# Kernel tuning notes

Hardware: AMD Instinct MI355X
Metric: run time of the kernel (lower is better)

Reference implementation:

```python
import jax, jax.numpy as jnp
import numpy as np

D_MODEL = 1024
NUM_HEADS = 16
HEAD_DIM = D_MODEL // NUM_HEADS


def setup_inputs() -> dict:
    key = jax.random.key(0)
    ks = jax.random.split(key, 5)
    scale = 1.0 / np.sqrt(D_MODEL)
    x = jax.random.normal(ks[0], (2, 2048, D_MODEL), dtype=jnp.float32)
    Wqkv = jax.random.normal(ks[1], (D_MODEL, 3 * D_MODEL), dtype=jnp.float32) * scale
    bqkv = jax.random.normal(ks[2], (3 * D_MODEL,), dtype=jnp.float32) * 0.02
    Wout = jax.random.normal(ks[3], (D_MODEL, D_MODEL), dtype=jnp.float32) * scale
    bout = jax.random.normal(ks[4], (D_MODEL,), dtype=jnp.float32) * 0.02
    return {"x": x, "Wqkv": Wqkv, "bqkv": bqkv, "Wout": Wout, "bout": bout}


def reference(x, Wqkv, bqkv, Wout, bout):
    B, T, D = x.shape
    H, Hd = NUM_HEADS, HEAD_DIM
    # fused QKV projection: [B,T,3D] -> [3,B,H,T,Hd]
    qkv = (x @ Wqkv + bqkv).reshape(B, T, 3, H, Hd).transpose(2, 0, 3, 1, 4)
    q, k, v = qkv[0], qkv[1], qkv[2]
    # scaled dot-product attention with full TxT scores (faithful to source)
    scores = jnp.einsum("bhqd,bhkd->bhqk", q, k) / np.sqrt(Hd).astype(np.float32)
    weights = jax.nn.softmax(scores, axis=-1)
    context = jnp.einsum("bhqk,bhkd->bhqd", weights, v)
    context = context.transpose(0, 2, 1, 3).reshape(B, T, D)
    return context @ Wout + bout
```

## Files before the change

kernel.cpp:

```cpp
#include <hip/hip_runtime.h>
#include <hip/hip_bf16.h>

#define D_MODEL 1024
#define T_SEQ   2048
#define BATCH   2
#define NHEADS  16
#define HDIM    64
#define QKVSZ   (BATCH * NHEADS * T_SEQ * HDIM)

#define SCALE_Q 0.18033688011112042f

typedef __bf16 bf16_t;
typedef bf16_t bf16x8  __attribute__((ext_vector_type(8)));
typedef float  f32x4   __attribute__((ext_vector_type(4)));
typedef float  f32x16  __attribute__((ext_vector_type(16)));
typedef unsigned uint32x4 __attribute__((ext_vector_type(4)));

#if __has_builtin(__builtin_amdgcn_exp2f)
#define EXP2F(x) __builtin_amdgcn_exp2f(x)
#else
#define EXP2F(x) exp2f(x)
#endif

__device__ __forceinline__ unsigned short f2bf(float f) {
    union { float f; unsigned u; } v; v.f = f;
    unsigned u = v.u;
    u += 0x7FFFu + ((u >> 16) & 1u);
    return (unsigned short)(u >> 16);
}

__device__ __forceinline__ unsigned pkbf(float a, float b) {
    unsigned r;
    asm("v_cvt_pk_bf16_f32 %0, %1, %2" : "=v"(r) : "v"(a), "v"(b));
    return r;
}

__device__ __forceinline__ void gload16(const unsigned short* g, unsigned short* l) {
    __builtin_amdgcn_global_load_lds(
        (const __attribute__((address_space(1))) void*)g,
        (__attribute__((address_space(3))) void*)l,
        16, 0, 0);
}

__global__ void cvt_f32_bf16(const float* __restrict__ src,
                             unsigned short* __restrict__ dst, int n4) {
    int i = blockIdx.x * blockDim.x + threadIdx.x;
    if (i < n4) {
        float4 v = reinterpret_cast<const float4*>(src)[i];
        ushort4 o;
        o.x = f2bf(v.x); o.y = f2bf(v.y); o.z = f2bf(v.z); o.w = f2bf(v.w);
        reinterpret_cast<ushort4*>(dst)[i] = o;
    }
}

__global__ __launch_bounds__(256) void cvt_transpose(
    const float* __restrict__ src, unsigned short* __restrict__ dst, int K, int N)
{
    __shared__ unsigned short Ls[64][72];
    const int n0 = blockIdx.x * 64, k0 = blockIdx.y * 64;
    const int tid = threadIdx.x;
    #pragma unroll
    for (int it = 0; it < 4; ++it) {
        const int r = it * 16 + (tid >> 4);
        const int c = (tid & 15) * 4;
        float4 v = *reinterpret_cast<const float4*>(src + (size_t)(k0 + r) * N + n0 + c);
        Ls[c + 0][r] = f2bf(v.x); Ls[c + 1][r] = f2bf(v.y);
        Ls[c + 2][r] = f2bf(v.z); Ls[c + 3][r] = f2bf(v.w);
    }
    __syncthreads();
    #pragma unroll
    for (int it = 0; it < 2; ++it) {
        const int rn = it * 32 + (tid >> 3);
        const int ck = (tid & 7) * 8;
        *reinterpret_cast<uint4*>(dst + (size_t)(n0 + rn) * K + k0 + ck) =
            *reinterpret_cast<const uint4*>(&Ls[rn][ck]);
    }
}

__global__ __launch_bounds__(256) void transpose_v(
    const unsigned short* __restrict__ v, unsigned short* __restrict__ vt)
{
    __shared__ unsigned short Ls[64][72];
    const int t0 = blockIdx.x * 64;
    const size_t base = ((size_t)(blockIdx.z * NHEADS + blockIdx.y)) * T_SEQ * HDIM;
    const int tid = threadIdx.x;
    const int r  = tid >> 2;
    const int c0 = (tid & 3) * 16;
    unsigned short tmp[16];
    *reinterpret_cast<uint4*>(&tmp[0]) =
        *reinterpret_cast<const uint4*>(v + base + (size_t)(t0 + r) * HDIM + c0);
    *reinterpret_cast<uint4*>(&tmp[8]) =
        *reinterpret_cast<const uint4*>(v + base + (size_t)(t0 + r) * HDIM + c0 + 8);
    #pragma unroll
    for (int i = 0; i < 16; ++i) Ls[c0 + i][r] = tmp[i];
    __syncthreads();
    const int rn = tid >> 2;
    const int ck = (tid & 3) * 16;
    const int a  = ck >> 4;
    const int kb = 32 * (a >> 1) + 16 * (a & 1);
    unsigned short buf[16];
    #pragma unroll
    for (int i = 0; i < 16; ++i) {
        const int key = kb + 4 * (i >> 3) + 8 * ((i & 7) >> 2) + (i & 3);
        buf[i] = Ls[rn][key];
    }
    *reinterpret_cast<uint4*>(vt + base + (size_t)rn * T_SEQ + t0 + ck) =
        *reinterpret_cast<const uint4*>(&buf[0]);
    *reinterpret_cast<uint4*>(vt + base + (size_t)rn * T_SEQ + t0 + ck + 8) =
        *reinterpret_cast<const uint4*>(&buf[8]);
}

template<int MODE>
__global__ __launch_bounds__(256) void gemm128(
    const unsigned short* __restrict__ A,
    const unsigned short* __restrict__ BT,
    const float* __restrict__ bias,
    unsigned short* __restrict__ qkv,
    float* __restrict__ outf,
    int M, int N, int K)
{
    __shared__ unsigned short As[2][128 * 32];
    __shared__ unsigned short Bs[2][128 * 32];
    const int tid = threadIdx.x, wv = tid >> 6, lane = tid & 63;
    const int wr = wv >> 1, wc = wv & 1;
    const int m0 = blockIdx.y * 128, n0 = blockIdx.x * 128;

    const int srow0 = 32 * wv + (lane >> 2);
    const int skc0  = (lane & 3) ^ ((srow0 >> 1) & 3);
    const int srow1 = srow0 + 16;
    const int skc1  = (lane & 3) ^ ((srow1 >> 1) & 3);

    #define GSTAGE(k0v, bf)                                                     \
        {                                                                       \
            gload16(A  + (size_t)(m0 + srow0) * K + (k0v) + skc0 * 8,           \
                    &As[bf][(32 * wv) * 32]);                                   \
            gload16(BT + (size_t)(n0 + srow0) * K + (k0v) + skc0 * 8,           \
                    &Bs[bf][(32 * wv) * 32]);                                   \
            gload16(A  + (size_t)(m0 + srow1) * K + (k0v) + skc1 * 8,           \
                    &As[bf][(32 * wv + 16) * 32]);                              \
            gload16(BT + (size_t)(n0 + srow1) * K + (k0v) + skc1 * 8,           \
                    &Bs[bf][(32 * wv + 16) * 32]);                              \
        }

    f32x4 acc[4][4] = {};

    GSTAGE(0, 0);
    __syncthreads();

    const int nk = K >> 5;
    for (int k = 0; k < nk; ++k) {
        const int cur = k & 1;
        if (k + 1 < nk) GSTAGE((k + 1) << 5, cur ^ 1);

        bf16x8 af[4], bfr[4];
        #pragma unroll
        for (int m = 0; m < 4; ++m) {
            const int row = 64 * wr + 16 * m + (lane & 15);
            const int s   = (lane >> 4) ^ ((row >> 1) & 3);
            af[m] = *reinterpret_cast<const bf16x8*>(&As[cur][row * 32 + s * 8]);
        }
        #pragma unroll
        for (int n = 0; n < 4; ++n) {
            const int row = 64 * wc + 16 * n + (lane & 15);
            const int s   = (lane >> 4) ^ ((row >> 1) & 3);
            bfr[n] = *reinterpret_cast<const bf16x8*>(&Bs[cur][row * 32 + s * 8]);
        }
        #pragma unroll
        for (int m = 0; m < 4; ++m)
            #pragma unroll
            for (int n = 0; n < 4; ++n)
                acc[m][n] = __builtin_amdgcn_mfma_f32_16x16x32_bf16(af[m], bfr[n], acc[m][n], 0, 0, 0);
        __syncthreads();
    }
    #undef GSTAGE

    const int rb = m0 + 64 * wr + ((lane >> 4) << 2);
    const int cb = n0 + 64 * wc + (lane & 15);
    #pragma unroll
    for (int n = 0; n < 4; ++n) {
        const int c = cb + 16 * n;
        const float bc = bias[c];
        #pragma unroll
        for (int m = 0; m < 4; ++m) {
            #pragma unroll
            for (int jr = 0; jr < 4; ++jr) {
                const int r = rb + 16 * m + jr;
                float val = acc[m][n][jr] + bc;
                if (MODE == 0) {
                    const int which = c >> 10;
                    const int rem = c & 1023;
                    const int h = rem >> 6, hd = rem & 63;
                    const int b = r >> 11, t = r & 2047;
                    if (which == 0) val *= SCALE_Q;
                    qkv[(size_t)which * QKVSZ + ((((size_t)b * NHEADS + h) * T_SEQ + t) << 6) + hd] = f2bf(val);
                } else {
                    outf[(size_t)r * N + c] = val;
                }
            }
        }
    }
}

__global__ __launch_bounds__(512) void attn32(
    const unsigned short* __restrict__ qb,
    const unsigned short* __restrict__ kb,
    const unsigned short* __restrict__ vtb,
    unsigned short* __restrict__ ctx)
{
    __shared__ unsigned short Ks[2][2][64 * 64];
    __shared__ unsigned short Vt[2][2][64 * 64];

    const int tid = threadIdx.x;
    const int wv = tid >> 6, lane = tid & 63;
    const int wg = wv >> 2, wl = wv & 3;
    const int ql = lane & 31;
    const int hi = lane >> 5;

    const int P    = blockIdx.x + 16 * blockIdx.y + 256 * blockIdx.z;
    const int xcd  = P & 7, slot = P >> 3;
    const int qt   = slot & 15;
    const int hidx = xcd * 4 + (slot >> 4);
    const int h    = hidx & 15, b = hidx >> 4;

    const size_t base = ((size_t)(b * NHEADS + h)) * T_SEQ * HDIM;
    const unsigned short* Kp  = kb  + base;
    const unsigned short* Vtp = vtb + base;
    const unsigned short* Qp  = qb  + base + ((size_t)qt * 128 + wl * 32 + ql) * HDIM;

    const bf16x8 qf0 = *reinterpret_cast<const bf16x8*>(Qp + 0  + hi * 8);
    const bf16x8 qf1 = *reinterpret_cast<const bf16x8*>(Qp + 16 + hi * 8);
    const bf16x8 qf2 = *reinterpret_cast<const bf16x8*>(Qp + 32 + hi * 8);
    const bf16x8 qf3 = *reinterpret_cast<const bf16x8*>(Qp + 48 + hi * 8);

    const int srow = lane >> 3;
    const int ssl  = lane & 7;
    #define STAGE(i, bf)                                                          \
        {                                                                         \
            _Pragma("unroll")                                                     \
            for (int ihalf = 0; ihalf < 2; ++ihalf) {                             \
                const int g2  = wl * 2 + ihalf;                                   \
                const int row = 8 * g2 + srow;                                    \
                const int sl  = ssl ^ (row & 7) ^ ((row >> 3) & 3);               \
                gload16(Kp  + (size_t)((wg * 16 + (i)) * 64 + row) * HDIM + sl * 8, \
                        &Ks[wg][bf][g2 * 512]);                                   \
                gload16(Vtp + (size_t)row * T_SEQ + (wg * 16 + (i)) * 64 + sl * 8, \
                        &Vt[wg][bf][g2 * 512]);                                   \
            }                                                                     \
        }

    STAGE(0, 0);
    __syncthreads();

    const int kx = (ql & 7) ^ ((ql >> 3) & 3);

    float m = -1e30f, l = 0.f;
    f32x16 o0 = {}, o1 = {};

    for (int i = 0; i < 16; ++i) {
        const int cur = i & 1;
        if (i + 1 < 16) STAGE(i + 1, cur ^ 1);

        f32x16 s0 = {}, s1 = {};
        __builtin_amdgcn_s_setprio(1);
        #pragma unroll
        for (int c = 0; c < 4; ++c) {
            const int sw = (2 * c + hi) ^ kx;
            const bf16x8 k0 = *reinterpret_cast<const bf16x8*>(&Ks[wg][cur][(ql)      * 64 + sw * 8]);
            const bf16x8 k1 = *reinterpret_cast<const bf16x8*>(&Ks[wg][cur][(32 + ql) * 64 + sw * 8]);
            const bf16x8 qc = (c == 0) ? qf0 : (c == 1) ? qf1 : (c == 2) ? qf2 : qf3;
            s0 = __builtin_amdgcn_mfma_f32_32x32x16_bf16(k0, qc, s0, 0, 0, 0);
            s1 = __builtin_amdgcn_mfma_f32_32x32x16_bf16(k1, qc, s1, 0, 0, 0);
        }
        __builtin_amdgcn_s_setprio(0);

        float a0 = fmaxf(s0[0], s0[4]), a1 = fmaxf(s0[1], s0[5]);
        float a2 = fmaxf(s0[2], s0[6]), a3 = fmaxf(s0[3], s0[7]);
        a0 = fmaxf(a0, fmaxf(s0[8],  s0[12]));  a1 = fmaxf(a1, fmaxf(s0[9],  s0[13]));
        a2 = fmaxf(a2, fmaxf(s0[10], s0[14])); a3 = fmaxf(a3, fmaxf(s0[11], s0[15]));
        a0 = fmaxf(a0, fmaxf(s1[0], s1[4]));   a1 = fmaxf(a1, fmaxf(s1[1], s1[5]));
        a2 = fmaxf(a2, fmaxf(s1[2], s1[6]));   a3 = fmaxf(a3, fmaxf(s1[3], s1[7]));
        a0 = fmaxf(a0, fmaxf(s1[8],  s1[12])); a1 = fmaxf(a1, fmaxf(s1[9],  s1[13]));
        a2 = fmaxf(a2, fmaxf(s1[10], s1[14])); a3 = fmaxf(a3, fmaxf(s1[11], s1[15]));
        float mx = fmaxf(fmaxf(a0, a1), fmaxf(a2, a3));
        mx = fmaxf(mx, __shfl_xor(mx, 32));

        if (__any(mx > m + 8.0f)) {
            const float mn = fmaxf(m, mx);
            const float sc = EXP2F(m - mn);
            l *= sc; m = mn;
            #pragma unroll
            for (int r = 0; r < 16; ++r) { o0[r] *= sc; o1[r] *= sc; }
        }

        #pragma unroll
        for (int r = 0; r < 16; ++r) s0[r] = EXP2F(s0[r] - m);
        #pragma unroll
        for (int r = 0; r < 16; ++r) s1[r] = EXP2F(s1[r] - m);
        float b0 = 0.f, b1 = 0.f, b2 = 0.f, b3 = 0.f;
        #pragma unroll
        for (int r = 0; r < 16; r += 4) {
            b0 += s0[r]; b1 += s0[r + 1]; b2 += s0[r + 2]; b3 += s0[r + 3];
            b0 += s1[r]; b1 += s1[r + 1]; b2 += s1[r + 2]; b3 += s1[r + 3];
        }
        float rs = (b0 + b1) + (b2 + b3);
        l += rs + __shfl_xor(rs, 32);

        __builtin_amdgcn_s_setprio(1);
        #pragma unroll
        for (int kc = 0; kc < 4; ++kc) {
            uint32x4 fw;
            if (kc == 0) {
                fw.x = pkbf(s0[0], s0[1]);   fw.y = pkbf(s0[2], s0[3]);
                fw.z = pkbf(s0[4], s0[5]);   fw.w = pkbf(s0[6], s0[7]);
            } else if (kc == 1) {
                fw.x = pkbf(s0[8], s0[9]);   fw.y = pkbf(s0[10], s0[11]);
                fw.z = pkbf(s0[12], s0[13]); fw.w = pkbf(s0[14], s0[15]);
            } else if (kc == 2) {
                fw.x = pkbf(s1[0], s1[1]);   fw.y = pkbf(s1[2], s1[3]);
                fw.z = pkbf(s1[4], s1[5]);   fw.w = pkbf(s1[6], s1[7]);
            } else {
                fw.x = pkbf(s1[8], s1[9]);   fw.y = pkbf(s1[10], s1[11]);
                fw.z = pkbf(s1[12], s1[13]); fw.w = pkbf(s1[14], s1[15]);
            }
            const bf16x8 pa = __builtin_bit_cast(bf16x8, fw);
            const int sw = (2 * kc + hi) ^ kx;
            const bf16x8 vva = *reinterpret_cast<const bf16x8*>(&Vt[wg][cur][(ql)      * 64 + sw * 8]);
            const bf16x8 vvb = *reinterpret_cast<const bf16x8*>(&Vt[wg][cur][(32 + ql) * 64 + sw * 8]);
            o0 = __builtin_amdgcn_mfma_f32_32x32x16_bf16(vva, pa, o0, 0, 0, 0);
            o1 = __builtin_amdgcn_mfma_f32_32x32x16_bf16(vvb, pa, o1, 0, 0, 0);
        }
        __builtin_amdgcn_s_setprio(0);

        __syncthreads();
    }
    #undef STAGE

    float* xo0  = (float*)&Ks[0][0][0];
    float* xo1m = (float*)&Vt[0][0][0];
    const int idx = wl * 64 + lane;
    if (wg == 1) {
        float* pa0 = xo0 + idx * 17;
        float* pb0 = xo1m + idx * 19;
        #pragma unroll
        for (int r = 0; r < 16; ++r) pa0[r] = o0[r];
        #pragma unroll
        for (int r = 0; r < 16; ++r) pb0[r] = o1[r];
        pb0[16] = m; pb0[17] = l;
    }
    __syncthreads();
    if (wg == 0) {
        const float* pa0 = xo0 + idx * 17;
        const float* pb0 = xo1m + idx * 19;
        const float m2 = pb0[16], l2 = pb0[17];
        const float mn = fmaxf(m, m2);
        const float ca = EXP2F(m - mn), cb = EXP2F(m2 - mn);
        const float invl = 1.0f / (l * ca + l2 * cb);
        const float fa = ca * invl, fb = cb * invl;

        const int t = qt * 128 + wl * 32 + ql;
        unsigned short* crow = ctx + ((size_t)b * T_SEQ + t) * D_MODEL + h * HDIM;
        #pragma unroll
        for (int r4 = 0; r4 < 4; ++r4) {
            const int d0 = 8 * r4 + 4 * hi;
            ushort4 w;
            w.x = f2bf(o0[4 * r4 + 0] * fa + pa0[4 * r4 + 0] * fb);
            w.y = f2bf(o0[4 * r4 + 1] * fa + pa0[4 * r4 + 1] * fb);
            w.z = f2bf(o0[4 * r4 + 2] * fa + pa0[4 * r4 + 2] * fb);
            w.w = f2bf(o0[4 * r4 + 3] * fa + pa0[4 * r4 + 3] * fb);
            *reinterpret_cast<ushort4*>(crow + d0) = w;
            w.x = f2bf(o1[4 * r4 + 0] * fa + pb0[4 * r4 + 0] * fb);
            w.y = f2bf(o1[4 * r4 + 1] * fa + pb0[4 * r4 + 1] * fb);
            w.z = f2bf(o1[4 * r4 + 2] * fa + pb0[4 * r4 + 2] * fb);
            w.w = f2bf(o1[4 * r4 + 3] * fa + pb0[4 * r4 + 3] * fb);
            *reinterpret_cast<ushort4*>(crow + 32 + d0) = w;
        }
    }
}

extern "C" void kernel_launch(void* const* d_in, const int* in_sizes, int n_in,
                              void* d_out, int out_size, void* d_ws, size_t ws_size,
                              hipStream_t stream) {
    const float* x    = (const float*)d_in[0];
    const float* Wqkv = (const float*)d_in[1];
    const float* bqkv = (const float*)d_in[2];
    const float* Wout = (const float*)d_in[3];
    const float* bout = (const float*)d_in[4];
    float* out = (float*)d_out;

    char* ws = (char*)d_ws;
    unsigned short* xb    = (unsigned short*)(ws);
    unsigned short* wqkvT = (unsigned short*)(ws + 8388608);
    unsigned short* woutT = (unsigned short*)(ws + 14680064);
    unsigned short* qkv   = (unsigned short*)(ws + 16777216);
    unsigned short* ctx   = (unsigned short*)(ws + 41943040);

    int n4 = (BATCH * T_SEQ * D_MODEL) / 4;
    cvt_f32_bf16<<<(n4 + 255) / 256, 256, 0, stream>>>(x, xb, n4);

    dim3 gt1(3 * D_MODEL / 64, D_MODEL / 64);
    cvt_transpose<<<gt1, 256, 0, stream>>>(Wqkv, wqkvT, D_MODEL, 3 * D_MODEL);
    dim3 gt2(D_MODEL / 64, D_MODEL / 64);
    cvt_transpose<<<gt2, 256, 0, stream>>>(Wout, woutT, D_MODEL, D_MODEL);

    dim3 g1(3 * D_MODEL / 128, (BATCH * T_SEQ) / 128);
    gemm128<0><<<g1, 256, 0, stream>>>(xb, wqkvT, bqkv, qkv, nullptr,
                                       BATCH * T_SEQ, 3 * D_MODEL, D_MODEL);

    dim3 gtv(T_SEQ / 64, NHEADS, BATCH);
    transpose_v<<<gtv, 256, 0, stream>>>(qkv + (size_t)2 * QKVSZ, xb);

    dim3 g2(T_SEQ / 128, NHEADS, BATCH);
    attn32<<<g2, 512, 0, stream>>>(qkv,
                                   qkv + (size_t)QKVSZ,
                                   xb,
                                   ctx);

    dim3 g3(D_MODEL / 128, (BATCH * T_SEQ) / 128);
    gemm128<1><<<g3, 256, 0, stream>>>(ctx, woutT, bout, nullptr, out,
                                       BATCH * T_SEQ, D_MODEL, D_MODEL);
}
```

Measured before the change: 130.9 us.

## Software-pipeline QK and softmax across iterations with staggered wave groups

The attention loop is restructured so the QK^T MFMA for the next key tile overlaps the softmax and PV of the current tile. K is prefetched two tiles ahead and V one tile ahead, and the two wave groups run softmax and QK in opposite orders so MFMA and VALU work interleave. Q is now staged in shared memory instead of held in registers, and the launch bound asks for 4 blocks per CU. This aims to hide softmax latency behind matrix work, at the cost of extra LDS traffic for Q and more register pressure from the double score buffers.

```diff
diff --git a/kernel.cpp b/kernel.cpp
--- a/kernel.cpp
+++ b/kernel.cpp
@@ -201,7 +201,7 @@
     }
 }
 
-__global__ __launch_bounds__(512) void attn32(
+__global__ __launch_bounds__(512, 4) void attn32(
     const unsigned short* __restrict__ qb,
     const unsigned short* __restrict__ kb,
     const unsigned short* __restrict__ vtb,
@@ -209,6 +209,7 @@
 {
     __shared__ unsigned short Ks[2][2][64 * 64];
     __shared__ unsigned short Vt[2][2][64 * 64];
+    __shared__ unsigned short Qs[128 * 64];
 
     const int tid = threadIdx.x;
     const int wv = tid >> 6, lane = tid & 63;
@@ -225,115 +226,154 @@
     const size_t base = ((size_t)(b * NHEADS + h)) * T_SEQ * HDIM;
     const unsigned short* Kp  = kb  + base;
     const unsigned short* Vtp = vtb + base;
-    const unsigned short* Qp  = qb  + base + ((size_t)qt * 128 + wl * 32 + ql) * HDIM;
-
-    const bf16x8 qf0 = *reinterpret_cast<const bf16x8*>(Qp + 0  + hi * 8);
-    const bf16x8 qf1 = *reinterpret_cast<const bf16x8*>(Qp + 16 + hi * 8);
-    const bf16x8 qf2 = *reinterpret_cast<const bf16x8*>(Qp + 32 + hi * 8);
-    const bf16x8 qf3 = *reinterpret_cast<const bf16x8*>(Qp + 48 + hi * 8);
+    const unsigned short* Qt  = qb  + base + (size_t)qt * 128 * HDIM;
 
     const int srow = lane >> 3;
     const int ssl  = lane & 7;
-    #define STAGE(i, bf)                                                          \
+
+    #define STAGE_K(i, bf)                                                        \
         {                                                                         \
             _Pragma("unroll")                                                     \
             for (int ihalf = 0; ihalf < 2; ++ihalf) {                             \
                 const int g2  = wl * 2 + ihalf;                                   \
                 const int row = 8 * g2 + srow;                                    \
                 const int sl  = ssl ^ (row & 7) ^ ((row >> 3) & 3);               \
-                gload16(Kp  + (size_t)((wg * 16 + (i)) * 64 + row) * HDIM + sl * 8, \
+                gload16(Kp + (size_t)((wg * 16 + (i)) * 64 + row) * HDIM + sl * 8,\
                         &Ks[wg][bf][g2 * 512]);                                   \
-                gload16(Vtp + (size_t)row * T_SEQ + (wg * 16 + (i)) * 64 + sl * 8, \
+            }                                                                     \
+        }
+    #define STAGE_V(i, bf)                                                        \
+        {                                                                         \
+            _Pragma("unroll")                                                     \
+            for (int ihalf = 0; ihalf < 2; ++ihalf) {                             \
+                const int g2  = wl * 2 + ihalf;                                   \
+                const int row = 8 * g2 + srow;                                    \
+                const int sl  = ssl ^ (row & 7) ^ ((row >> 3) & 3);               \
+                gload16(Vtp + (size_t)row * T_SEQ + (wg * 16 + (i)) * 64 + sl * 8,\
                         &Vt[wg][bf][g2 * 512]);                                   \
             }                                                                     \
         }
 
-    STAGE(0, 0);
+    {
+        #pragma unroll
+        for (int ihalf = 0; ihalf < 2; ++ihalf) {
+            const int g2  = wv * 2 + ihalf;
+            const int row = 8 * g2 + srow;
+            const int sl  = ssl ^ (row & 7) ^ ((row >> 3) & 3);
+            gload16(Qt + (size_t)row * HDIM + sl * 8, &Qs[g2 * 512]);
+        }
+    }
+    STAGE_K(0, 0); STAGE_V(0, 0); STAGE_K(1, 1);
     __syncthreads();
 
     const int kx = (ql & 7) ^ ((ql >> 3) & 3);
 
+    #define QK_MFMA(SOUT0, SOUT1, NXT)                                            \
+        {                                                                         \
+            __builtin_amdgcn_s_setprio(1);                                        \
+            _Pragma("unroll")                                                     \
+            for (int c = 0; c < 4; ++c) {                                         \
+                const int sw = (2 * c + hi) ^ kx;                                 \
+                const bf16x8 k0 = *reinterpret_cast<const bf16x8*>(&Ks[wg][NXT][(ql)      * 64 + sw * 8]); \
+                const bf16x8 k1 = *reinterpret_cast<const bf16x8*>(&Ks[wg][NXT][(32 + ql) * 64 + sw * 8]); \
+                const bf16x8 qc = *reinterpret_cast<const bf16x8*>(&Qs[(wl * 32 + ql) * 64 + sw * 8]);     \
+                SOUT0 = __builtin_amdgcn_mfma_f32_32x32x16_bf16(k0, qc, SOUT0, 0, 0, 0); \
+                SOUT1 = __builtin_amdgcn_mfma_f32_32x32x16_bf16(k1, qc, SOUT1, 0, 0, 0); \
+            }                                                                     \
+            __builtin_amdgcn_s_setprio(0);                                        \
+        }
+
+    #define SOFTMAX_PACK(SIN0, SIN1)                                             \
+        {                                                                         \
+            float a0 = fmaxf(SIN0[0], SIN0[4]), a1 = fmaxf(SIN0[1], SIN0[5]);     \
+            float a2 = fmaxf(SIN0[2], SIN0[6]), a3 = fmaxf(SIN0[3], SIN0[7]);     \
+            a0 = fmaxf(a0, fmaxf(SIN0[8],  SIN0[12])); a1 = fmaxf(a1, fmaxf(SIN0[9],  SIN0[13])); \
+            a2 = fmaxf(a2, fmaxf(SIN0[10], SIN0[14])); a3 = fmaxf(a3, fmaxf(SIN0[11], SIN0[15])); \
+            a0 = fmaxf(a0, fmaxf(SIN1[0], SIN1[4]));   a1 = fmaxf(a1, fmaxf(SIN1[1], SIN1[5]));   \
+            a2 = fmaxf(a2, fmaxf(SIN1[2], SIN1[6]));   a3 = fmaxf(a3, fmaxf(SIN1[3], SIN1[7]));   \
+            a0 = fmaxf(a0, fmaxf(SIN1[8],  SIN1[12])); a1 = fmaxf(a1, fmaxf(SIN1[9],  SIN1[13])); \
+            a2 = fmaxf(a2, fmaxf(SIN1[10], SIN1[14])); a3 = fmaxf(a3, fmaxf(SIN1[11], SIN1[15])); \
+            float mx = fmaxf(fmaxf(a0, a1), fmaxf(a2, a3));                       \
+            mx = fmaxf(mx, __shfl_xor(mx, 32));                                   \
+            if (__any(mx > m + 8.0f)) {                                           \
+                const float mn = fmaxf(m, mx);                                    \
+                const float sc = EXP2F(m - mn);                                   \
+                l *= sc; m = mn;                                                  \
+                _Pragma("unroll")                                                 \
+                for (int r = 0; r < 16; ++r) { o0[r] *= sc; o1[r] *= sc; }        \
+            }                                                                     \
+            _Pragma("unroll")                                                     \
+            for (int r = 0; r < 16; ++r) SIN0[r] = EXP2F(SIN0[r] - m);            \
+            _Pragma("unroll")                                                     \
+            for (int r = 0; r < 16; ++r) SIN1[r] = EXP2F(SIN1[r] - m);            \
+            float b0 = 0.f, b1 = 0.f, b2 = 0.f, b3 = 0.f;                         \
+            _Pragma("unroll")                                                     \
+            for (int r = 0; r < 16; r += 4) {                                     \
+                b0 += SIN0[r]; b1 += SIN0[r + 1]; b2 += SIN0[r + 2]; b3 += SIN0[r + 3]; \
+                b0 += SIN1[r]; b1 += SIN1[r + 1]; b2 += SIN1[r + 2]; b3 += SIN1[r + 3]; \
+            }                                                                     \
+            float rs = (b0 + b1) + (b2 + b3);                                     \
+            l += rs + __shfl_xor(rs, 32);                                         \
+            pwa.x = pkbf(SIN0[0], SIN0[1]);   pwa.y = pkbf(SIN0[2], SIN0[3]);     \
+            pwa.z = pkbf(SIN0[4], SIN0[5]);   pwa.w = pkbf(SIN0[6], SIN0[7]);     \
+            pwb.x = pkbf(SIN0[8], SIN0[9]);   pwb.y = pkbf(SIN0[10], SIN0[11]);   \
+            pwb.z = pkbf(SIN0[12], SIN0[13]); pwb.w = pkbf(SIN0[14], SIN0[15]);   \
+            pwc.x = pkbf(SIN1[0], SIN1[1]);   pwc.y = pkbf(SIN1[2], SIN1[3]);     \
+            pwc.z = pkbf(SIN1[4], SIN1[5]);   pwc.w = pkbf(SIN1[6], SIN1[7]);     \
+            pwd.x = pkbf(SIN1[8], SIN1[9]);   pwd.y = pkbf(SIN1[10], SIN1[11]);   \
+            pwd.z = pkbf(SIN1[12], SIN1[13]); pwd.w = pkbf(SIN1[14], SIN1[15]);   \
+        }
+
+    #define PV_STEP(PW, KC, CUR)                                                  \
+        {                                                                         \
+            const bf16x8 pa = __builtin_bit_cast(bf16x8, PW);                     \
+            const int sw = (2 * (KC) + hi) ^ kx;                                  \
+            const bf16x8 vva = *reinterpret_cast<const bf16x8*>(&Vt[wg][CUR][(ql)      * 64 + sw * 8]); \
+            const bf16x8 vvb = *reinterpret_cast<const bf16x8*>(&Vt[wg][CUR][(32 + ql) * 64 + sw * 8]); \
+            o0 = __builtin_amdgcn_mfma_f32_32x32x16_bf16(vva, pa, o0, 0, 0, 0);   \
+            o1 = __builtin_amdgcn_mfma_f32_32x32x16_bf16(vvb, pa, o1, 0, 0, 0);   \
+        }
+    #define PV_MFMA(CUR)                                                          \
+        {                                                                         \
+            __builtin_amdgcn_s_setprio(1);                                        \
+            PV_STEP(pwa, 0, CUR); PV_STEP(pwb, 1, CUR);                           \
+            PV_STEP(pwc, 2, CUR); PV_STEP(pwd, 3, CUR);                           \
+            __builtin_amdgcn_s_setprio(0);                                        \
+        }
+
     float m = -1e30f, l = 0.f;
-    f32x16 o0 = {}, o1 = {};
-
-    for (int i = 0; i < 16; ++i) {
-        const int cur = i & 1;
-        if (i + 1 < 16) STAGE(i + 1, cur ^ 1);
-
-        f32x16 s0 = {}, s1 = {};
-        __builtin_amdgcn_s_setprio(1);
-        #pragma unroll
-        for (int c = 0; c < 4; ++c) {
-            const int sw = (2 * c + hi) ^ kx;
-            const bf16x8 k0 = *reinterpret_cast<const bf16x8*>(&Ks[wg][cur][(ql)      * 64 + sw * 8]);
-            const bf16x8 k1 = *reinterpret_cast<const bf16x8*>(&Ks[wg][cur][(32 + ql) * 64 + sw * 8]);
-            const bf16x8 qc = (c == 0) ? qf0 : (c == 1) ? qf1 : (c == 2) ? qf2 : qf3;
-            s0 = __builtin_amdgcn_mfma_f32_32x32x16_bf16(k0, qc, s0, 0, 0, 0);
-            s1 = __builtin_amdgcn_mfma_f32_32x32x16_bf16(k1, qc, s1, 0, 0, 0);
-        }
-        __builtin_amdgcn_s_setprio(0);
-
-        float a0 = fmaxf(s0[0], s0[4]), a1 = fmaxf(s0[1], s0[5]);
-        float a2 = fmaxf(s0[2], s0[6]), a3 = fmaxf(s0[3], s0[7]);
-        a0 = fmaxf(a0, fmaxf(s0[8],  s0[12]));  a1 = fmaxf(a1, fmaxf(s0[9],  s0[13]));
-        a2 = fmaxf(a2, fmaxf(s0[10], s0[14])); a3 = fmaxf(a3, fmaxf(s0[11], s0[15]));
-        a0 = fmaxf(a0, fmaxf(s1[0], s1[4]));   a1 = fmaxf(a1, fmaxf(s1[1], s1[5]));
-        a2 = fmaxf(a2, fmaxf(s1[2], s1[6]));   a3 = fmaxf(a3, fmaxf(s1[3], s1[7]));
-        a0 = fmaxf(a0, fmaxf(s1[8],  s1[12])); a1 = fmaxf(a1, fmaxf(s1[9],  s1[13]));
-        a2 = fmaxf(a2, fmaxf(s1[10], s1[14])); a3 = fmaxf(a3, fmaxf(s1[11], s1[15]));
-        float mx = fmaxf(fmaxf(a0, a1), fmaxf(a2, a3));
-        mx = fmaxf(mx, __shfl_xor(mx, 32));
-
-        if (__any(mx > m + 8.0f)) {
-            const float mn = fmaxf(m, mx);
-            const float sc = EXP2F(m - mn);
-            l *= sc; m = mn;
-            #pragma unroll
-            for (int r = 0; r < 16; ++r) { o0[r] *= sc; o1[r] *= sc; }
-        }
-
-        #pragma unroll
-        for (int r = 0; r < 16; ++r) s0[r] = EXP2F(s0[r] - m);
-        #pragma unroll
-        for (int r = 0; r < 16; ++r) s1[r] = EXP2F(s1[r] - m);
-        float b0 = 0.f, b1 = 0.f, b2 = 0.f, b3 = 0.f;
-        #pragma unroll
-        for (int r = 0; r < 16; r += 4) {
-            b0 += s0[r]; b1 += s0[r + 1]; b2 += s0[r + 2]; b3 += s0[r + 3];
-            b0 += s1[r]; b1 += s1[r + 1]; b2 += s1[r + 2]; b3 += s1[r + 3];
-        }
-        float rs = (b0 + b1) + (b2 + b3);
-        l += rs + __shfl_xor(rs, 32);
-
-        __builtin_amdgcn_s_setprio(1);
-        #pragma unroll
-        for (int kc = 0; kc < 4; ++kc) {
-            uint32x4 fw;
-            if (kc == 0) {
-                fw.x = pkbf(s0[0], s0[1]);   fw.y = pkbf(s0[2], s0[3]);
-                fw.z = pkbf(s0[4], s0[5]);   fw.w = pkbf(s0[6], s0[7]);
-            } else if (kc == 1) {
-                fw.x = pkbf(s0[8], s0[9]);   fw.y = pkbf(s0[10], s0[11]);
-                fw.z = pkbf(s0[12], s0[13]); fw.w = pkbf(s0[14], s0[15]);
-            } else if (kc == 2) {
-                fw.x = pkbf(s1[0], s1[1]);   fw.y = pkbf(s1[2], s1[3]);
-                fw.z = pkbf(s1[4], s1[5]);   fw.w = pkbf(s1[6], s1[7]);
-            } else {
-                fw.x = pkbf(s1[8], s1[9]);   fw.y = pkbf(s1[10], s1[11]);
-                fw.z = pkbf(s1[12], s1[13]); fw.w = pkbf(s1[14], s1[15]);
-            }
-            const bf16x8 pa = __builtin_bit_cast(bf16x8, fw);
-            const int sw = (2 * kc + hi) ^ kx;
-            const bf16x8 vva = *reinterpret_cast<const bf16x8*>(&Vt[wg][cur][(ql)      * 64 + sw * 8]);
-            const bf16x8 vvb = *reinterpret_cast<const bf16x8*>(&Vt[wg][cur][(32 + ql) * 64 + sw * 8]);
-            o0 = __builtin_amdgcn_mfma_f32_32x32x16_bf16(vva, pa, o0, 0, 0, 0);
-            o1 = __builtin_amdgcn_mfma_f32_32x32x16_bf16(vvb, pa, o1, 0, 0, 0);
-        }
-        __builtin_amdgcn_s_setprio(0);
-
-        __syncthreads();
-    }
-    #undef STAGE
+    f32x16 o0 = (f32x16)0.0f, o1 = (f32x16)0.0f;
+    f32x16 sA0 = (f32x16)0.0f, sA1 = (f32x16)0.0f;
+    f32x16 sB0, sB1;
+
+    QK_MFMA(sA0, sA1, 0);
+    __syncthreads();
+
+    #define ITER(I, CUR, NXT, SI0, SI1, SO0, SO1)                                 \
+        {                                                                         \
+            if ((I) + 1 < 16) STAGE_V((I) + 1, NXT);                              \
+            if ((I) + 2 < 16) STAGE_K((I) + 2, CUR);                              \
+            SO0 = (f32x16)0.0f; SO1 = (f32x16)0.0f;                               \
+            uint32x4 pwa, pwb, pwc, pwd;                                          \
+            if (wg) {                                                             \
+                if ((I) + 1 < 16) QK_MFMA(SO0, SO1, NXT);                         \
+                SOFTMAX_PACK(SI0, SI1);                                           \
+                PV_MFMA(CUR);                                                     \
+            } else {                                                              \
+                SOFTMAX_PACK(SI0, SI1);                                           \
+                if ((I) + 1 < 16) QK_MFMA(SO0, SO1, NXT);                         \
+                PV_MFMA(CUR);                                                     \
+            }                                                                     \
+            __syncthreads();                                                      \
+        }
+
+    for (int i = 0; i < 16; i += 2) {
+        ITER(i,     0, 1, sA0, sA1, sB0, sB1);
+        ITER(i + 1, 1, 0, sB0, sB1, sA0, sA1);
+    }
+    #undef ITER
+    #undef STAGE_K
+    #undef STAGE_V
 
     float* xo0  = (float*)&Ks[0][0][0];
     float* xo1m = (float*)&Vt[0][0][0];
```

After: 205.5 us. 57.1% more time.
